# Optimization experiments

Measured on AMD Instinct MI355X. Metric: run time of the kernel, lower is better.

Reference implementation:

```python
import jax, jax.numpy as jnp
import numpy as np

EPS = 1e-5

def _layer_norm(x, w, b):
    mu = jnp.mean(x, axis=-1, keepdims=True)
    var = jnp.mean((x - mu) ** 2, axis=-1, keepdims=True)
    return (x - mu) * jax.lax.rsqrt(var + EPS) * w + b

def setup_inputs() -> dict:
    H = 2048
    B, T = 4, 2048
    key = jax.random.key(0)
    ks = jax.random.split(key, 12)
    s = 0.02
    return {
        "hidden_state": jax.random.normal(ks[0], (B, T, H), dtype=jnp.float32),
        "ln_w": jnp.ones((H,), jnp.float32),
        "ln_b": jnp.zeros((H,), jnp.float32),
        "Wk": jax.random.normal(ks[1], (H, H), jnp.float32) * s,
        "Wv": jax.random.normal(ks[2], (H, H), jnp.float32) * s,
        "Wr": jax.random.normal(ks[3], (H, H), jnp.float32) * s,
        "Wo": jax.random.normal(ks[4], (H, H), jnp.float32) * s,
        "mix_k": jax.random.uniform(ks[5], (H,), jnp.float32),
        "mix_v": jax.random.uniform(ks[6], (H,), jnp.float32),
        "mix_r": jax.random.uniform(ks[7], (H,), jnp.float32),
        "time_decay": jax.random.normal(ks[8], (H,), jnp.float32) * 0.5,
        "current_token_weight": jax.random.normal(ks[9], (H,), jnp.float32) * 0.5,
    }

def _wkv(k, v, time_decay, curr_w):
    # k, v: [B, T, H]; max-stabilized RWKV recurrence, scanned over time.
    B, T, H = k.shape
    decay = -jnp.exp(time_decay)  # [H]
    num0 = jnp.zeros((B, H), k.dtype)
    den0 = jnp.zeros((B, H), k.dtype)
    norm0 = jnp.full((B, H), -jnp.inf, k.dtype)

    def step(carry, kv):
        num, den, norm = carry
        kt, vt = kv  # [B, H]
        ct = curr_w + kt
        cn = jnp.maximum(ct, norm)
        e_prev = jnp.exp(norm - cn)
        e_cur = jnp.exp(ct - cn)
        out = (e_prev * num + e_cur * vt) / (e_prev * den + e_cur)
        dpn = decay + norm
        new_norm = jnp.maximum(dpn, kt)
        e_d = jnp.exp(dpn - new_norm)
        e_k = jnp.exp(kt - new_norm)
        return (e_d * num + e_k * vt, e_d * den + e_k, new_norm), out

    kT = jnp.swapaxes(k, 0, 1)  # [T, B, H]
    vT = jnp.swapaxes(v, 0, 1)
    (num, den, norm), outs = jax.lax.scan(step, (num0, den0, norm0), (kT, vT))
    return jnp.swapaxes(outs, 0, 1), num, den, norm

def reference(hidden_state, ln_w, ln_b, Wk, Wv, Wr, Wo, mix_k, mix_v, mix_r,
              time_decay, current_token_weight):
    residual = hidden_state
    x = _layer_norm(hidden_state, ln_w, ln_b)  # [B, T, H]
    B, T, H = x.shape
    # shifted input: previous token (zeros for t=0 since previous_state is None)
    sx = jnp.concatenate([jnp.zeros((B, 1, H), x.dtype), x[:, :-1, :]], axis=1)
    xk = sx + mix_k * (x - sx)
    xv = sx + mix_v * (x - sx)
    xr = sx + mix_r * (x - sx)
    r = jax.nn.sigmoid(jnp.einsum('bth,oh->bto', xr, Wr))
    k = jnp.einsum('bth,oh->bto', xk, Wk)
    v = jnp.einsum('bth,oh->bto', xv, Wv)
    wkv, num, den, norm = _wkv(k, v, time_decay, current_token_weight)
    rwkv = jnp.einsum('bth,oh->bto', r * wkv, Wo)
    out = residual + rwkv
    return (out, (x[:, -1, :], num, den, norm))
```

## Files before the change

kernel.cpp:

```cpp
#include <hip/hip_runtime.h>
#include <hip/hip_bf16.h>
#include <stdint.h>

#define B_ 4
#define T_ 2048
#define H_ 2048
#define BT_ (B_ * T_)
#define BH_ (B_ * H_)
#define CH_ 32
#define CL_ (T_ / CH_)
#define NKT_ (H_ / 64)

typedef __bf16 bf16x8 __attribute__((ext_vector_type(8)));
typedef float f32x4 __attribute__((ext_vector_type(4)));

__device__ inline void async16(const void* g, void* l) {
  __builtin_amdgcn_global_load_lds(
      (__attribute__((address_space(1))) uint32_t*)(void*)(uintptr_t)g,
      (__attribute__((address_space(3))) uint32_t*)l,
      16, 0, 0);
}

__global__ __launch_bounds__(256) void cvt_bf16_kernel(
    const float* __restrict__ w0, const float* __restrict__ w1,
    const float* __restrict__ w2, const float* __restrict__ w3,
    __bf16* __restrict__ dst ) {
  const float* srcs[4] = {w0, w1, w2, w3};
  const float* src = srcs[blockIdx.y];
  __bf16* d = dst + (size_t)blockIdx.y * H_ * H_;
  int i = (blockIdx.x * 256 + threadIdx.x) * 8;
  const float4* s4 = (const float4*)(src + i);
  float4 a = s4[0], b = s4[1];
  bf16x8 o;
  o[0] = (__bf16)a.x; o[1] = (__bf16)a.y; o[2] = (__bf16)a.z; o[3] = (__bf16)a.w;
  o[4] = (__bf16)b.x; o[5] = (__bf16)b.y; o[6] = (__bf16)b.z; o[7] = (__bf16)b.w;
  *(bf16x8*)(d + i) = o;
}

__global__ __launch_bounds__(256) void ln_mix_kernel(
    const float* __restrict__ h, const float* __restrict__ lnw,
    const float* __restrict__ lnb, const float* __restrict__ mk,
    const float* __restrict__ mv, const float* __restrict__ mr,
    __bf16* __restrict__ xk, __bf16* __restrict__ xv, __bf16* __restrict__ xr,
    float* __restrict__ xlast) {
  const int row = blockIdx.x;
  const int t = row & (T_ - 1);
  const int tid = threadIdx.x;
  const bool hasprev = (t != 0);

  const float4* cr = (const float4*)(h + (size_t)row * H_);
  float4 c0 = cr[tid * 2 + 0], c1 = cr[tid * 2 + 1];
  float4 p0 = {0.f, 0.f, 0.f, 0.f}, p1 = {0.f, 0.f, 0.f, 0.f};
  if (hasprev) {
    const float4* pr = (const float4*)(h + (size_t)(row - 1) * H_);
    p0 = pr[tid * 2 + 0]; p1 = pr[tid * 2 + 1];
  }
  float4 red;
  red.x = c0.x + c0.y + c0.z + c0.w + c1.x + c1.y + c1.z + c1.w;
  red.y = c0.x * c0.x + c0.y * c0.y + c0.z * c0.z + c0.w * c0.w +
          c1.x * c1.x + c1.y * c1.y + c1.z * c1.z + c1.w * c1.w;
  red.z = p0.x + p0.y + p0.z + p0.w + p1.x + p1.y + p1.z + p1.w;
  red.w = p0.x * p0.x + p0.y * p0.y + p0.z * p0.z + p0.w * p0.w +
          p1.x * p1.x + p1.y * p1.y + p1.z * p1.z + p1.w * p1.w;
  #pragma unroll
  for (int off = 32; off; off >>= 1) {
    red.x += __shfl_down(red.x, off);
    red.y += __shfl_down(red.y, off);
    red.z += __shfl_down(red.z, off);
    red.w += __shfl_down(red.w, off);
  }
  __shared__ float4 rbuf_[4];
  const int lane = tid & 63, wid = tid >> 6;
  if (lane == 0) rbuf_[wid] = red;
  __syncthreads();
  float4 tot;
  tot.x = rbuf_[0].x + rbuf_[1].x + rbuf_[2].x + rbuf_[3].x;
  tot.y = rbuf_[0].y + rbuf_[1].y + rbuf_[2].y + rbuf_[3].y;
  tot.z = rbuf_[0].z + rbuf_[1].z + rbuf_[2].z + rbuf_[3].z;
  tot.w = rbuf_[0].w + rbuf_[1].w + rbuf_[2].w + rbuf_[3].w;

  const float inv = 1.0f / (float)H_;
  float mu = tot.x * inv;
  float rstd = rsqrtf(fmaxf(tot.y * inv - mu * mu, 0.f) + 1e-5f);
  float mup = tot.z * inv;
  float rstdp = rsqrtf(fmaxf(tot.w * inv - mup * mup, 0.f) + 1e-5f);

  float xc[8] = {c0.x, c0.y, c0.z, c0.w, c1.x, c1.y, c1.z, c1.w};
  float xp[8] = {p0.x, p0.y, p0.z, p0.w, p1.x, p1.y, p1.z, p1.w};
  const float4* W4 = (const float4*)lnw;
  const float4* Bv4 = (const float4*)lnb;
  const float4* MK4 = (const float4*)mk;
  const float4* MV4 = (const float4*)mv;
  const float4* MR4 = (const float4*)mr;
  float4 w0 = W4[tid * 2], w1 = W4[tid * 2 + 1];
  float4 b0 = Bv4[tid * 2], b1 = Bv4[tid * 2 + 1];
  float4 k0 = MK4[tid * 2], k1 = MK4[tid * 2 + 1];
  float4 v0 = MV4[tid * 2], v1 = MV4[tid * 2 + 1];
  float4 r0 = MR4[tid * 2], r1 = MR4[tid * 2 + 1];
  float wa[8] = {w0.x, w0.y, w0.z, w0.w, w1.x, w1.y, w1.z, w1.w};
  float ba[8] = {b0.x, b0.y, b0.z, b0.w, b1.x, b1.y, b1.z, b1.w};
  float ka[8] = {k0.x, k0.y, k0.z, k0.w, k1.x, k1.y, k1.z, k1.w};
  float va[8] = {v0.x, v0.y, v0.z, v0.w, v1.x, v1.y, v1.z, v1.w};
  float ra[8] = {r0.x, r0.y, r0.z, r0.w, r1.x, r1.y, r1.z, r1.w};

  bf16x8 ok_, ov_, or_;
  float xls[8];
  #pragma unroll
  for (int e = 0; e < 8; e++) {
    float x = (xc[e] - mu) * rstd * wa[e] + ba[e];
    float sx = hasprev ? (xp[e] - mup) * rstdp * wa[e] + ba[e] : 0.f;
    ok_[e] = (__bf16)(sx + ka[e] * (x - sx));
    ov_[e] = (__bf16)(sx + va[e] * (x - sx));
    or_[e] = (__bf16)(sx + ra[e] * (x - sx));
    xls[e] = x;
  }
  size_t obase = (size_t)row * H_ + tid * 8;
  *(bf16x8*)(xk + obase) = ok_;
  *(bf16x8*)(xv + obase) = ov_;
  *(bf16x8*)(xr + obase) = or_;
  if (t == T_ - 1) {
    float* dst = xlast + (size_t)(row >> 11) * H_ + tid * 8;
    #pragma unroll
    for (int e = 0; e < 8; e++) dst[e] = xls[e];
  }
}

__global__ __launch_bounds__(256, 2) void gemm_kvr(
    const __bf16* __restrict__ A0, const __bf16* __restrict__ A1,
    const __bf16* __restrict__ A2, const __bf16* __restrict__ Wb,
    __bf16* __restrict__ o0, __bf16* __restrict__ o1, __bf16* __restrict__ o2) {
  __shared__ __align__(16) char ring[2][32768];

  const int wgid = blockIdx.x;
  const int z = wgid >> 10;
  const int g = wgid & 1023;
  const int x = g & 7;
  const int i = g >> 3;
  const int bm = x * 8 + (i & 7);
  const int bn = i >> 3;

  const __bf16* A = (z == 0) ? A0 : (z == 1 ? A1 : A2);
  const __bf16* Bw = Wb + (size_t)z * H_ * H_;
  __bf16* ob = (z == 0) ? o0 : (z == 1 ? o1 : o2);

  const int tid = threadIdx.x;
  const int lane = tid & 63, wv = tid >> 6;
  const int wm = wv >> 1;
  const int wn = wv & 1;
  const int rr = lane & 15, q = lane >> 4;

  f32x4 acc[4][4];
  #pragma unroll
  for (int m = 0; m < 4; m++)
    #pragma unroll
    for (int n = 0; n < 4; n++) acc[m][n] = (f32x4){0.f, 0.f, 0.f, 0.f};

  const char* Ag = (const char*)A + (size_t)(bm * 128) * (H_ * 2);
  const char* Bg = (const char*)Bw + (size_t)(bn * 128) * (H_ * 2);

  const int srow = wv * 8 + (lane >> 3);
  const int scol = ((lane & 7) ^ (lane >> 3)) << 4;
  const int rsw = rr & 7;

#define STAGE_TILE(kt_, buf_)                                                   \
  {                                                                             \
    char* base_ = ring[buf_];                                                   \
    _Pragma("unroll")                                                           \
    for (int mh_ = 0; mh_ < 2; mh_++) {                                         \
      const char* Mg_ = mh_ ? Bg : Ag;                                          \
      _Pragma("unroll")                                                         \
      for (int rd_ = 0; rd_ < 4; rd_++) {                                       \
        char* dst_ = base_ + mh_ * 16384 + rd_ * 4096 + wv * 1024;              \
        const char* src_ = Mg_ + (size_t)(rd_ * 32 + srow) * (H_ * 2)           \
                           + (kt_) * 128 + scol;                                \
        async16(src_, dst_);                                                    \
      }                                                                         \
    }                                                                           \
  }

  STAGE_TILE(0, 0);
  asm volatile("s_waitcnt vmcnt(0)" ::: "memory");
  __builtin_amdgcn_s_barrier();

  for (int kt = 0; kt < NKT_; kt++) {
    const int cur = kt & 1, nxt = cur ^ 1;
    const char* Alds = ring[cur];
    const char* Blds = ring[cur] + 16384;

    if (kt + 1 < NKT_) STAGE_TILE(kt + 1, nxt);

    bf16x8 bfr[4][2];
    #pragma unroll
    for (int ni = 0; ni < 4; ni++)
      #pragma unroll
      for (int ks = 0; ks < 2; ks++) {
        int row_t = wn * 64 + ni * 16 + rr;
        bfr[ni][ks] = *(const bf16x8*)(Blds + row_t * 128 +
                                       (((ks * 4 + q) ^ rsw) << 4));
      }

    __builtin_amdgcn_s_setprio(1);
    #pragma unroll
    for (int mi = 0; mi < 4; mi++) {
      bf16x8 af[2];
      #pragma unroll
      for (int ks = 0; ks < 2; ks++) {
        int row_t = wm * 64 + mi * 16 + rr;
        af[ks] = *(const bf16x8*)(Alds + row_t * 128 +
                                  (((ks * 4 + q) ^ rsw) << 4));
      }
      #pragma unroll
      for (int ks = 0; ks < 2; ks++)
        #pragma unroll
        for (int ni = 0; ni < 4; ni++)
          acc[mi][ni] = __builtin_amdgcn_mfma_f32_16x16x32_bf16(
              af[ks], bfr[ni][ks], acc[mi][ni], 0, 0, 0);
    }
    __builtin_amdgcn_s_setprio(0);

    if (kt + 1 < NKT_) {
      asm volatile("s_waitcnt vmcnt(0)" ::: "memory");
      __builtin_amdgcn_s_barrier();
    }
  }
#undef STAGE_TILE

  const int r0 = bm * 128 + wm * 64 + q * 4;
  const int c0 = bn * 128 + wn * 64 + rr;
  #pragma unroll
  for (int mi = 0; mi < 4; mi++) {
    #pragma unroll
    for (int ni = 0; ni < 4; ni++) {
      int col = c0 + ni * 16;
      #pragma unroll
      for (int rg = 0; rg < 4; rg++) {
        int rowg = r0 + mi * 16 + rg;
        size_t idx = (size_t)rowg * H_ + col;
        float vv = acc[mi][ni][rg];
        if (z == 2) {
          ob[idx] = (__bf16)(1.f / (1.f + __expf(-vv)));
        } else {
          ob[idx] = (__bf16)vv;
        }
      }
    }
  }
}

__global__ __launch_bounds__(512, 1) void gemm_wo(
    const __bf16* __restrict__ A, const __bf16* __restrict__ Bw,
    float* __restrict__ outf, const float* __restrict__ resid) {
  __shared__ __align__(16) char ring[2][65536];

  const int wgid = blockIdx.x;
  const int lin = (wgid & 7) * 32 + (wgid >> 3);
  const int bm = lin >> 3;
  const int bn = lin & 7;

  const int tid = threadIdx.x;
  const int lane = tid & 63, wv = tid >> 6;
  const int wm = wv >> 2;
  const int wn = wv & 3;
  const int rr = lane & 15, q = lane >> 4;

  f32x4 acc[8][4];
  #pragma unroll
  for (int m = 0; m < 8; m++)
    #pragma unroll
    for (int n = 0; n < 4; n++) acc[m][n] = (f32x4){0.f, 0.f, 0.f, 0.f};

  const char* Ag = (const char*)A + (size_t)(bm * 256) * (H_ * 2);
  const char* Bg = (const char*)Bw + (size_t)(bn * 256) * (H_ * 2);

  const int srow = wv * 8 + (lane >> 3);
  const int scol = ((lane & 7) ^ (lane >> 3)) << 4;
  const int rsw = rr & 7;

#define STAGE_TILE(kt_, buf_)                                                   \
  {                                                                             \
    char* base_ = ring[buf_];                                                   \
    _Pragma("unroll")                                                           \
    for (int mh_ = 0; mh_ < 2; mh_++) {                                         \
      const char* Mg_ = mh_ ? Bg : Ag;                                          \
      _Pragma("unroll")                                                         \
      for (int hh_ = 0; hh_ < 2; hh_++) {                                       \
        _Pragma("unroll")                                                       \
        for (int rd_ = 0; rd_ < 2; rd_++) {                                     \
          char* dst_ = base_ + mh_ * 32768 + hh_ * 16384 + rd_ * 8192 + wv * 1024; \
          const char* src_ = Mg_ + (size_t)(hh_ * 128 + rd_ * 64 + srow) * (H_ * 2) \
                             + (kt_) * 128 + scol;                              \
          async16(src_, dst_);                                                  \
        }                                                                       \
      }                                                                         \
    }                                                                           \
  }

  STAGE_TILE(0, 0);
  asm volatile("s_waitcnt vmcnt(0)" ::: "memory");
  __builtin_amdgcn_s_barrier();

  for (int kt = 0; kt < NKT_; kt++) {
    const int cur = kt & 1, nxt = cur ^ 1;
    const char* Alds = ring[cur];
    const char* Blds = ring[cur] + 32768;

    if (kt + 1 < NKT_) STAGE_TILE(kt + 1, nxt);

    bf16x8 bfr[4][2];
    #pragma unroll
    for (int ni = 0; ni < 4; ni++)
      #pragma unroll
      for (int ks = 0; ks < 2; ks++) {
        int row_t = wn * 64 + ni * 16 + rr;
        bfr[ni][ks] = *(const bf16x8*)(Blds + row_t * 128 +
                                       (((ks * 4 + q) ^ rsw) << 4));
      }

    #pragma unroll
    for (int p = 0; p < 4; p++) {
      bf16x8 af[2][2];
      #pragma unroll
      for (int mi = 0; mi < 2; mi++)
        #pragma unroll
        for (int ks = 0; ks < 2; ks++) {
          int row_t = wm * 128 + p * 32 + mi * 16 + rr;
          af[mi][ks] = *(const bf16x8*)(Alds + row_t * 128 +
                                        (((ks * 4 + q) ^ rsw) << 4));
        }
      #pragma unroll
      for (int ks = 0; ks < 2; ks++)
        #pragma unroll
        for (int mi = 0; mi < 2; mi++)
          #pragma unroll
          for (int ni = 0; ni < 4; ni++)
            acc[p * 2 + mi][ni] = __builtin_amdgcn_mfma_f32_16x16x32_bf16(
                af[mi][ks], bfr[ni][ks], acc[p * 2 + mi][ni], 0, 0, 0);
    }

    if (kt + 1 < NKT_) {
      asm volatile("s_waitcnt vmcnt(0)" ::: "memory");
      __builtin_amdgcn_s_barrier();
    }
  }
#undef STAGE_TILE

  const int r0 = bm * 256 + wm * 128 + q * 4;
  const int c0 = bn * 256 + wn * 64 + rr;
  #pragma unroll
  for (int m = 0; m < 8; m++) {
    #pragma unroll
    for (int n = 0; n < 4; n++) {
      int col = c0 + n * 16;
      #pragma unroll
      for (int rg = 0; rg < 4; rg++) {
        int rowg = r0 + m * 16 + rg;
        size_t idx = (size_t)rowg * H_ + col;
        outf[idx] = resid[idx] + acc[m][n][rg];
      }
    }
  }
}

__global__ __launch_bounds__(256) void wkv_pass1(
    const __bf16* __restrict__ k, const __bf16* __restrict__ v,
    const float* __restrict__ td,
    float* __restrict__ cs_num, float* __restrict__ cs_den,
    float* __restrict__ cs_norm) {
  const int id = blockIdx.x * 256 + threadIdx.x;
  const int c = blockIdx.y;
  const int b = id >> 11;
  const int hh = id & (H_ - 1);
  const float decay = -__expf(td[hh]);
  float num = 0.f, den = 0.f, norm = -INFINITY;

  const int UN = 16;
  for (int t0 = c * CL_; t0 < (c + 1) * CL_; t0 += UN) {
    float kk[UN], vv[UN];
    size_t base = ((size_t)b * T_ + t0) * H_ + hh;
    #pragma unroll
    for (int i = 0; i < UN; i++) {
      kk[i] = (float)k[base + (size_t)i * H_];
      vv[i] = (float)v[base + (size_t)i * H_];
    }
    #pragma unroll
    for (int i = 0; i < UN; i++) {
      float dpn = decay + norm;
      float nn = fmaxf(dpn, kk[i]);
      float ed = __expf(dpn - nn), ek = __expf(kk[i] - nn);
      num = ed * num + ek * vv[i];
      den = ed * den + ek;
      norm = nn;
    }
  }
  cs_num[c * BH_ + id] = num;
  cs_den[c * BH_ + id] = den;
  cs_norm[c * BH_ + id] = norm;
}

__global__ __launch_bounds__(256) void wkv_scan(
    const float* __restrict__ cs_num, const float* __restrict__ cs_den,
    const float* __restrict__ cs_norm, const float* __restrict__ td,
    float* __restrict__ px_num, float* __restrict__ px_den,
    float* __restrict__ px_norm) {
  const int id = blockIdx.x * 256 + threadIdx.x;
  const int hh = id & (H_ - 1);
  const float Lw = -__expf(td[hh]) * (float)CL_;
  float num = 0.f, den = 0.f, norm = -INFINITY;
  for (int c = 0; c < CH_; c++) {
    px_num[c * BH_ + id] = num;
    px_den[c * BH_ + id] = den;
    px_norm[c * BH_ + id] = norm;
    float n_c = cs_num[c * BH_ + id];
    float d_c = cs_den[c * BH_ + id];
    float m_c = cs_norm[c * BH_ + id];
    float sn = norm + Lw;
    float on = fmaxf(sn, m_c);
    float ea = __expf(sn - on), eb = __expf(m_c - on);
    num = ea * num + eb * n_c;
    den = ea * den + eb * d_c;
    norm = on;
  }
}

__global__ __launch_bounds__(256) void wkv_pass2(
    const __bf16* __restrict__ k, const __bf16* __restrict__ v,
    const __bf16* __restrict__ r, const float* __restrict__ td,
    const float* __restrict__ cw,
    const float* __restrict__ px_num, const float* __restrict__ px_den,
    const float* __restrict__ px_norm,
    __bf16* __restrict__ a, float* __restrict__ ndn) {
  const int id = blockIdx.x * 256 + threadIdx.x;
  const int c = blockIdx.y;
  const int b = id >> 11;
  const int hh = id & (H_ - 1);
  const float decay = -__expf(td[hh]);
  const float cwv = cw[hh];
  float num = px_num[c * BH_ + id];
  float den = px_den[c * BH_ + id];
  float norm = px_norm[c * BH_ + id];

  const int UN = 16;
  for (int t0 = c * CL_; t0 < (c + 1) * CL_; t0 += UN) {
    float kk[UN], vv[UN], rrv[UN];
    size_t base = ((size_t)b * T_ + t0) * H_ + hh;
    #pragma unroll
    for (int i = 0; i < UN; i++) {
      kk[i] = (float)k[base + (size_t)i * H_];
      vv[i] = (float)v[base + (size_t)i * H_];
      rrv[i] = (float)r[base + (size_t)i * H_];
    }
    #pragma unroll
    for (int i = 0; i < UN; i++) {
      float kt = kk[i], vt = vv[i];
      float ct = cwv + kt;
      float cn = fmaxf(ct, norm);
      float ep = __expf(norm - cn), ec = __expf(ct - cn);
      float o = (ep * num + ec * vt) / (ep * den + ec);
      a[base + (size_t)i * H_] = (__bf16)(rrv[i] * o);
      float dpn = decay + norm;
      float nn = fmaxf(dpn, kt);
      float ed = __expf(dpn - nn), ek = __expf(kt - nn);
      num = ed * num + ek * vt;
      den = ed * den + ek;
      norm = nn;
    }
  }
  if (c == CH_ - 1) {
    ndn[id] = num;
    ndn[BH_ + id] = den;
    ndn[2 * BH_ + id] = norm;
  }
}

extern "C" void kernel_launch(void* const* d_in, const int* in_sizes, int n_in,
                              void* d_out, int out_size, void* d_ws, size_t ws_size,
                              hipStream_t stream) {
  const float* h   = (const float*)d_in[0];
  const float* lnw = (const float*)d_in[1];
  const float* lnb = (const float*)d_in[2];
  const float* Wk  = (const float*)d_in[3];
  const float* Wv  = (const float*)d_in[4];
  const float* Wr  = (const float*)d_in[5];
  const float* Wo  = (const float*)d_in[6];
  const float* mk  = (const float*)d_in[7];
  const float* mv  = (const float*)d_in[8];
  const float* mr  = (const float*)d_in[9];
  const float* td  = (const float*)d_in[10];
  const float* cw  = (const float*)d_in[11];

  char* ws = (char*)d_ws;
  const size_t MB = 1048576;
  __bf16* xk   = (__bf16*)(ws);
  __bf16* xv   = (__bf16*)(ws + 32 * MB);
  __bf16* xr   = (__bf16*)(ws + 64 * MB);
  __bf16* kbuf = (__bf16*)(ws + 96 * MB);
  __bf16* vbuf = (__bf16*)(ws + 128 * MB);
  __bf16* W16  = (__bf16*)(ws + 160 * MB);
  __bf16* rbuf = (__bf16*)(ws + 192 * MB);
  __bf16* Wo16 = W16 + 3 * (size_t)H_ * H_;
  float* cs_num  = (float*)(ws + 64 * MB);
  float* cs_den  = cs_num + (size_t)CH_ * BH_;
  float* cs_norm = cs_den + (size_t)CH_ * BH_;
  float* px_num  = cs_norm + (size_t)CH_ * BH_;
  float* px_den  = px_num + (size_t)CH_ * BH_;
  float* px_norm = px_den + (size_t)CH_ * BH_;

  float* out  = (float*)d_out;
  float* xlast = out + (size_t)BT_ * H_;
  float* ndn   = xlast + (size_t)B_ * H_;

  dim3 cg((H_ * H_) / (256 * 8), 4);
  cvt_bf16_kernel<<<cg, 256, 0, stream>>>(Wk, Wv, Wr, Wo, W16);

  ln_mix_kernel<<<BT_, 256, 0, stream>>>(h, lnw, lnb, mk, mv, mr, xk, xv, xr, xlast);

  gemm_kvr<<<3072, 256, 0, stream>>>(xk, xv, xr, W16, kbuf, vbuf, rbuf);

  dim3 wg(BH_ / 256, CH_);
  wkv_pass1<<<wg, 256, 0, stream>>>(kbuf, vbuf, td, cs_num, cs_den, cs_norm);
  wkv_scan<<<BH_ / 256, 256, 0, stream>>>(cs_num, cs_den, cs_norm, td,
                                          px_num, px_den, px_norm);
  wkv_pass2<<<wg, 256, 0, stream>>>(kbuf, vbuf, rbuf, td, cw,
                                    px_num, px_den, px_norm,
                                    xk , ndn);

  gemm_wo<<<256, 512, 0, stream>>>(xk, Wo16, out, h);
}
```

Measured before the change: 379.8 us.

## Shrink Wo GEMM tile to 128x128 with two blocks per CU

Replaces the 256x256, 512-thread output-projection GEMM with a 128x128 tile kernel of 256 threads, launched as 1024 blocks with two resident per CU. LDS use per block drops to 64KB and the block-index mapping is regrouped for L2 locality. The MFMA section is also wrapped in s_setprio. The aim is better occupancy and tail balance on the 256-CU device, at the cost of lower per-tile data reuse and more global/LDS traffic per FLOP.

```diff
diff --git a/kernel.cpp b/kernel.cpp
--- a/kernel.cpp
+++ b/kernel.cpp
@@ -247,30 +247,31 @@
   }
 }
 
-__global__ __launch_bounds__(512, 1) void gemm_wo(
+__global__ __launch_bounds__(256, 2) void gemm_wo128(
     const __bf16* __restrict__ A, const __bf16* __restrict__ Bw,
     float* __restrict__ outf, const float* __restrict__ resid) {
-  __shared__ __align__(16) char ring[2][65536];
-
-  const int wgid = blockIdx.x;
-  const int lin = (wgid & 7) * 32 + (wgid >> 3);
-  const int bm = lin >> 3;
-  const int bn = lin & 7;
+  __shared__ __align__(16) char ring[2][32768];
+
+  const int g = blockIdx.x;
+  const int x = g & 7;
+  const int i = g >> 3;
+  const int bm = x * 8 + (i & 7);
+  const int bn = i >> 3;
 
   const int tid = threadIdx.x;
   const int lane = tid & 63, wv = tid >> 6;
-  const int wm = wv >> 2;
-  const int wn = wv & 3;
+  const int wm = wv >> 1;
+  const int wn = wv & 1;
   const int rr = lane & 15, q = lane >> 4;
 
-  f32x4 acc[8][4];
+  f32x4 acc[4][4];
   #pragma unroll
-  for (int m = 0; m < 8; m++)
+  for (int m = 0; m < 4; m++)
     #pragma unroll
     for (int n = 0; n < 4; n++) acc[m][n] = (f32x4){0.f, 0.f, 0.f, 0.f};
 
-  const char* Ag = (const char*)A + (size_t)(bm * 256) * (H_ * 2);
-  const char* Bg = (const char*)Bw + (size_t)(bn * 256) * (H_ * 2);
+  const char* Ag = (const char*)A + (size_t)(bm * 128) * (H_ * 2);
+  const char* Bg = (const char*)Bw + (size_t)(bn * 128) * (H_ * 2);
 
   const int srow = wv * 8 + (lane >> 3);
   const int scol = ((lane & 7) ^ (lane >> 3)) << 4;
@@ -283,14 +284,11 @@
     for (int mh_ = 0; mh_ < 2; mh_++) {                                         \
       const char* Mg_ = mh_ ? Bg : Ag;                                          \
       _Pragma("unroll")                                                         \
-      for (int hh_ = 0; hh_ < 2; hh_++) {                                       \
-        _Pragma("unroll")                                                       \
-        for (int rd_ = 0; rd_ < 2; rd_++) {                                     \
-          char* dst_ = base_ + mh_ * 32768 + hh_ * 16384 + rd_ * 8192 + wv * 1024; \
-          const char* src_ = Mg_ + (size_t)(hh_ * 128 + rd_ * 64 + srow) * (H_ * 2) \
-                             + (kt_) * 128 + scol;                              \
-          async16(src_, dst_);                                                  \
-        }                                                                       \
+      for (int rd_ = 0; rd_ < 4; rd_++) {                                       \
+        char* dst_ = base_ + mh_ * 16384 + rd_ * 4096 + wv * 1024;              \
+        const char* src_ = Mg_ + (size_t)(rd_ * 32 + srow) * (H_ * 2)           \
+                           + (kt_) * 128 + scol;                                \
+        async16(src_, dst_);                                                    \
       }                                                                         \
     }                                                                           \
   }
@@ -302,7 +300,7 @@
   for (int kt = 0; kt < NKT_; kt++) {
     const int cur = kt & 1, nxt = cur ^ 1;
     const char* Alds = ring[cur];
-    const char* Blds = ring[cur] + 32768;
+    const char* Blds = ring[cur] + 16384;
 
     if (kt + 1 < NKT_) STAGE_TILE(kt + 1, nxt);
 
@@ -316,26 +314,24 @@
                                        (((ks * 4 + q) ^ rsw) << 4));
       }
 
-    #pragma unroll
-    for (int p = 0; p < 4; p++) {
-      bf16x8 af[2][2];
-      #pragma unroll
-      for (int mi = 0; mi < 2; mi++)
-        #pragma unroll
-        for (int ks = 0; ks < 2; ks++) {
-          int row_t = wm * 128 + p * 32 + mi * 16 + rr;
-          af[mi][ks] = *(const bf16x8*)(Alds + row_t * 128 +
-                                        (((ks * 4 + q) ^ rsw) << 4));
-        }
+    __builtin_amdgcn_s_setprio(1);
+    #pragma unroll
+    for (int mi = 0; mi < 4; mi++) {
+      bf16x8 af[2];
+      #pragma unroll
+      for (int ks = 0; ks < 2; ks++) {
+        int row_t = wm * 64 + mi * 16 + rr;
+        af[ks] = *(const bf16x8*)(Alds + row_t * 128 +
+                                  (((ks * 4 + q) ^ rsw) << 4));
+      }
       #pragma unroll
       for (int ks = 0; ks < 2; ks++)
         #pragma unroll
-        for (int mi = 0; mi < 2; mi++)
-          #pragma unroll
-          for (int ni = 0; ni < 4; ni++)
-            acc[p * 2 + mi][ni] = __builtin_amdgcn_mfma_f32_16x16x32_bf16(
-                af[mi][ks], bfr[ni][ks], acc[p * 2 + mi][ni], 0, 0, 0);
-    }
+        for (int ni = 0; ni < 4; ni++)
+          acc[mi][ni] = __builtin_amdgcn_mfma_f32_16x16x32_bf16(
+              af[ks], bfr[ni][ks], acc[mi][ni], 0, 0, 0);
+    }
+    __builtin_amdgcn_s_setprio(0);
 
     if (kt + 1 < NKT_) {
       asm volatile("s_waitcnt vmcnt(0)" ::: "memory");
@@ -344,18 +340,18 @@
   }
 #undef STAGE_TILE
 
-  const int r0 = bm * 256 + wm * 128 + q * 4;
-  const int c0 = bn * 256 + wn * 64 + rr;
+  const int r0 = bm * 128 + wm * 64 + q * 4;
+  const int c0 = bn * 128 + wn * 64 + rr;
   #pragma unroll
-  for (int m = 0; m < 8; m++) {
-    #pragma unroll
-    for (int n = 0; n < 4; n++) {
-      int col = c0 + n * 16;
+  for (int mi = 0; mi < 4; mi++) {
+    #pragma unroll
+    for (int ni = 0; ni < 4; ni++) {
+      int col = c0 + ni * 16;
       #pragma unroll
       for (int rg = 0; rg < 4; rg++) {
-        int rowg = r0 + m * 16 + rg;
+        int rowg = r0 + mi * 16 + rg;
         size_t idx = (size_t)rowg * H_ + col;
-        outf[idx] = resid[idx] + acc[m][n][rg];
+        outf[idx] = resid[idx] + acc[mi][ni][rg];
       }
     }
   }
@@ -524,5 +520,5 @@
                                     px_num, px_den, px_norm,
                                     xk , ndn);
 
-  gemm_wo<<<256, 512, 0, stream>>>(xk, Wo16, out, h);
-}
+  gemm_wo128<<<1024, 256, 0, stream>>>(xk, Wo16, out, h);
+}
```

Result: slower. 389.5 us (+2.5%).
